# Performance work log

Hardware: AMD Instinct MI355X
Metric: run time of the kernel (lower is better)

Reference implementation:

```python
import jax, jax.numpy as jnp
import numpy as np

B, C, H, W = 32, 256, 64, 64
K = 7  # kernel_size

def setup_inputs() -> dict:
    key = jax.random.key(0)
    kx, kw = jax.random.split(key)
    x = jax.random.normal(kx, (B, C, H, W), dtype=jnp.float32)
    # Conv2d(2, 1, 7, bias=False) weight: [out_ch=1, in_ch=2, 7, 7]
    w = jax.random.normal(kw, (1, 2, K, K), dtype=jnp.float32) * (1.0 / np.sqrt(2 * K * K))
    return {"x": x, "w": w}

def reference(x, w):
    # channel-wise max and mean, keepdim -> [B,1,H,W]
    max_out = jnp.max(x, axis=1, keepdims=True)
    avg_out = jnp.mean(x, axis=1, keepdims=True)
    concat = jnp.concatenate([max_out, avg_out], axis=1)  # [B,2,H,W]
    pad = K // 2
    conv = jax.lax.conv_general_dilated(
        concat, w,
        window_strides=(1, 1),
        padding=[(pad, pad), (pad, pad)],
        dimension_numbers=("NCHW", "OIHW", "NCHW"),
    )  # [B,1,H,W]
    scale = jax.nn.sigmoid(conv)
    return x * scale  # broadcast over channels
```

## Files before the change

kernel.cpp:

```cpp
#include <hip/hip_runtime.h>
#include <math.h>

constexpr int Bn  = 32;
constexpr int Cn  = 256;
constexpr int Hn  = 64;
constexpr int Wn  = 64;
constexpr int HW  = Hn * Wn;
constexpr int CHW = Cn * HW;
constexpr int HW4 = HW / 4;
constexpr int NPOS  = Bn * HW;
constexpr int NPOS4 = NPOS / 4;

constexpr int ROWS   = 16;
constexpr int NSTR   = Hn / ROWS;
constexpr int CGRP   = 16;
constexpr int NCG    = Cn / CGRP;
constexpr int HALO   = 3;
constexpr int LROWS  = ROWS + 2 * HALO;

__global__ __launch_bounds__(256) void reduce_k(const float* __restrict__ x,
                                                float* __restrict__ pmax,
                                                float* __restrict__ pavg) {
    __shared__ float4 smax[4][64];
    __shared__ float4 ssum[4][64];

    const int lane  = threadIdx.x & 63;
    const int chunk = threadIdx.x >> 6;
    const int pos4  = blockIdx.x * 64 + lane;
    const int b     = pos4 >> 10;
    const int sp4   = pos4 & (HW4 - 1);

    const float4* xp = (const float4*)x + (size_t)b * (CHW / 4)
                       + (size_t)(chunk * 64) * HW4 + sp4;

    float4 mx = make_float4(-INFINITY, -INFINITY, -INFINITY, -INFINITY);
    float4 sm = make_float4(0.f, 0.f, 0.f, 0.f);

    #pragma unroll 8
    for (int c = 0; c < 64; ++c) {
        float4 v = xp[(size_t)c * HW4];
        mx.x = fmaxf(mx.x, v.x); mx.y = fmaxf(mx.y, v.y);
        mx.z = fmaxf(mx.z, v.z); mx.w = fmaxf(mx.w, v.w);
        sm.x += v.x; sm.y += v.y; sm.z += v.z; sm.w += v.w;
    }

    smax[chunk][lane] = mx;
    ssum[chunk][lane] = sm;
    __syncthreads();

    if (chunk == 0) {
        float4 M = smax[0][lane];
        float4 S = ssum[0][lane];
        #pragma unroll
        for (int k = 1; k < 4; ++k) {
            float4 m2 = smax[k][lane];
            float4 s2 = ssum[k][lane];
            M.x = fmaxf(M.x, m2.x); M.y = fmaxf(M.y, m2.y);
            M.z = fmaxf(M.z, m2.z); M.w = fmaxf(M.w, m2.w);
            S.x += s2.x; S.y += s2.y; S.z += s2.z; S.w += s2.w;
        }
        const float inv = 1.0f / (float)Cn;
        float4 A = make_float4(S.x * inv, S.y * inv, S.z * inv, S.w * inv);
        ((float4*)pmax)[pos4] = M;
        ((float4*)pavg)[pos4] = A;
    }
}

__global__ __launch_bounds__(256, 8) void convmul_k(const float* __restrict__ x,
                                                    const float* __restrict__ pmax,
                                                    const float* __restrict__ pavg,
                                                    const float* __restrict__ w,
                                                    float* __restrict__ out) {
    __shared__ float spm[LROWS * Wn];
    __shared__ float spa[LROWS * Wn];
    __shared__ float ssc[ROWS * Wn];
    __shared__ float sw[98];

    const int tid = threadIdx.x;
    const int bid = blockIdx.x;
    const int cg     = bid & (NCG - 1);
    const int stripe = (bid >> 4) & (NSTR - 1);
    const int b      = bid >> 6;
    const int r0     = stripe * ROWS;

    if (tid < 98) sw[tid] = w[tid];

    const float* pm = pmax + b * HW;
    const float* pa = pavg + b * HW;
    for (int i = tid; i < LROWS * Wn; i += 256) {
        const int lr  = i >> 6;
        const int col = i & 63;
        const int gh  = r0 - HALO + lr;
        const bool ok = (gh >= 0) && (gh < Hn);
        spm[i] = ok ? pm[gh * Wn + col] : 0.f;
        spa[i] = ok ? pa[gh * Wn + col] : 0.f;
    }
    __syncthreads();

    #pragma unroll
    for (int p = tid; p < ROWS * Wn; p += 256) {
        const int hl  = p >> 6;
        const int col = p & 63;
        float acc = 0.f;
        #pragma unroll
        for (int kh = 0; kh < 7; ++kh) {
            const int lr = hl + kh;
            #pragma unroll
            for (int kw = 0; kw < 7; ++kw) {
                const int ww = col + kw - 3;
                if (ww < 0 || ww >= Wn) continue;
                const int o = lr * Wn + ww;
                acc += spm[o] * sw[kh * 7 + kw] + spa[o] * sw[49 + kh * 7 + kw];
            }
        }
        ssc[p] = 1.f / (1.f + expf(-acc));
    }
    __syncthreads();

    const float4 s = ((const float4*)ssc)[tid];

    const size_t base = (size_t)b * (CHW / 4)
                      + (size_t)(cg * CGRP) * HW4
                      + (size_t)stripe * (ROWS * Wn / 4) + tid;
    const float4* x4 = (const float4*)x;
    float4* o4 = (float4*)out;

    #pragma unroll 4
    for (int ch = 0; ch < CGRP; ++ch) {
        const size_t i4 = base + (size_t)ch * HW4;
        const float4 v = x4[i4];
        float4 o;
        o.x = v.x * s.x; o.y = v.y * s.y;
        o.z = v.z * s.z; o.w = v.w * s.w;
        o4[i4] = o;
    }
}

extern "C" void kernel_launch(void* const* d_in, const int* in_sizes, int n_in,
                              void* d_out, int out_size, void* d_ws, size_t ws_size,
                              hipStream_t stream) {
    const float* x = (const float*)d_in[0];
    const float* w = (const float*)d_in[1];
    float* out = (float*)d_out;

    float* pmax = (float*)d_ws;
    float* pavg = pmax + NPOS;

    reduce_k<<<NPOS4 / 64, 256, 0, stream>>>(x, pmax, pavg);

    convmul_k<<<Bn * NSTR * NCG, 256, 0, stream>>>(x, pmax, pavg, w, out);
}
```

Before: 277.5 us.

## Compute the spatial-attention conv once per position and scale all channels per block

The conv+multiply kernel is repartitioned. Each block now covers 4 rows of one image and all 256 channels, matching reduce_k's tiling, instead of a 16-row stripe times 16 channels. That removes the 16-fold redundant 7x7 conv and sigmoid work across channel groups. The shared-memory halo is padded in the column dimension so the conv loop drops its bounds checks, and output stores become nontemporal. The trade-off is a grid four times smaller with a longer serial channel loop per thread, which may cut the number of memory requests in flight.

```diff
diff --git a/kernel.cpp b/kernel.cpp
--- a/kernel.cpp
+++ b/kernel.cpp
@@ -11,12 +11,12 @@
 constexpr int NPOS  = Bn * HW;
 constexpr int NPOS4 = NPOS / 4;
 
-constexpr int ROWS   = 16;
-constexpr int NSTR   = Hn / ROWS;
-constexpr int CGRP   = 16;
-constexpr int NCG    = Cn / CGRP;
-constexpr int HALO   = 3;
-constexpr int LROWS  = ROWS + 2 * HALO;
+constexpr int CM_ROWS  = 4;
+constexpr int CM_LR    = CM_ROWS + 6;
+constexpr int CM_LC    = 72;
+constexpr int CM_GRID  = NPOS4 / 64;
+
+typedef float f4_t __attribute__((ext_vector_type(4)));
 
 __global__ __launch_bounds__(256) void reduce_k(const float* __restrict__ x,
                                                 float* __restrict__ pmax,
@@ -66,73 +66,72 @@
     }
 }
 
-__global__ __launch_bounds__(256, 8) void convmul_k(const float* __restrict__ x,
-                                                    const float* __restrict__ pmax,
-                                                    const float* __restrict__ pavg,
-                                                    const float* __restrict__ w,
-                                                    float* __restrict__ out) {
-    __shared__ float spm[LROWS * Wn];
-    __shared__ float spa[LROWS * Wn];
-    __shared__ float ssc[ROWS * Wn];
+__global__ __launch_bounds__(256) void convmul_k(const float* __restrict__ x,
+                                                 const float* __restrict__ pmax,
+                                                 const float* __restrict__ pavg,
+                                                 const float* __restrict__ w,
+                                                 float* __restrict__ out) {
+    __shared__ float spm[CM_LR][CM_LC];
+    __shared__ float spa[CM_LR][CM_LC];
+    __shared__ float ssc[256];
     __shared__ float sw[98];
 
     const int tid = threadIdx.x;
     const int bid = blockIdx.x;
-    const int cg     = bid & (NCG - 1);
-    const int stripe = (bid >> 4) & (NSTR - 1);
-    const int b      = bid >> 6;
-    const int r0     = stripe * ROWS;
+    const int b   = bid >> 4;
+    const int rg  = bid & 15;
+    const int row0 = rg * CM_ROWS;
 
     if (tid < 98) sw[tid] = w[tid];
 
     const float* pm = pmax + b * HW;
     const float* pa = pavg + b * HW;
-    for (int i = tid; i < LROWS * Wn; i += 256) {
-        const int lr  = i >> 6;
-        const int col = i & 63;
-        const int gh  = r0 - HALO + lr;
-        const bool ok = (gh >= 0) && (gh < Hn);
-        spm[i] = ok ? pm[gh * Wn + col] : 0.f;
-        spa[i] = ok ? pa[gh * Wn + col] : 0.f;
+    for (int i = tid; i < CM_LR * CM_LC; i += 256) {
+        const int lr = i / CM_LC;
+        const int lc = i % CM_LC;
+        const int gh = row0 - 3 + lr;
+        const int gw = lc - 3;
+        const bool ok = (gh >= 0) && (gh < Hn) && (gw >= 0) && (gw < Wn);
+        const float vm = ok ? pm[gh * Wn + gw] : 0.f;
+        const float va = ok ? pa[gh * Wn + gw] : 0.f;
+        spm[lr][lc] = vm;
+        spa[lr][lc] = va;
     }
     __syncthreads();
 
-    #pragma unroll
-    for (int p = tid; p < ROWS * Wn; p += 256) {
-        const int hl  = p >> 6;
-        const int col = p & 63;
+    {
+        const int hl  = tid >> 6;
+        const int col = tid & 63;
         float acc = 0.f;
         #pragma unroll
         for (int kh = 0; kh < 7; ++kh) {
-            const int lr = hl + kh;
             #pragma unroll
             for (int kw = 0; kw < 7; ++kw) {
-                const int ww = col + kw - 3;
-                if (ww < 0 || ww >= Wn) continue;
-                const int o = lr * Wn + ww;
-                acc += spm[o] * sw[kh * 7 + kw] + spa[o] * sw[49 + kh * 7 + kw];
+                acc += spm[hl + kh][col + kw] * sw[kh * 7 + kw]
+                     + spa[hl + kh][col + kw] * sw[49 + kh * 7 + kw];
             }
         }
-        ssc[p] = 1.f / (1.f + expf(-acc));
+        ssc[tid] = 1.f / (1.f + expf(-acc));
     }
     __syncthreads();
 
-    const float4 s = ((const float4*)ssc)[tid];
+    const int wv   = tid >> 6;
+    const int lane = tid & 63;
+    const int sp4  = rg * 64 + lane;
 
-    const size_t base = (size_t)b * (CHW / 4)
-                      + (size_t)(cg * CGRP) * HW4
-                      + (size_t)stripe * (ROWS * Wn / 4) + tid;
+    const float4 s = ((const float4*)ssc)[lane];
+
     const float4* x4 = (const float4*)x;
     float4* o4 = (float4*)out;
 
+    size_t idx = (size_t)b * (CHW / 4) + (size_t)(wv * 64) * HW4 + sp4;
     #pragma unroll 4
-    for (int ch = 0; ch < CGRP; ++ch) {
-        const size_t i4 = base + (size_t)ch * HW4;
-        const float4 v = x4[i4];
-        float4 o;
+    for (int k = 0; k < 64; ++k, idx += HW4) {
+        const float4 v = x4[idx];
+        f4_t o;
         o.x = v.x * s.x; o.y = v.y * s.y;
         o.z = v.z * s.z; o.w = v.w * s.w;
-        o4[i4] = o;
+        __builtin_nontemporal_store(o, (f4_t*)&o4[idx]);
     }
 }
 
@@ -148,5 +147,5 @@
 
     reduce_k<<<NPOS4 / 64, 256, 0, stream>>>(x, pmax, pavg);
 
-    convmul_k<<<Bn * NSTR * NCG, 256, 0, stream>>>(x, pmax, pavg, w, out);
+    convmul_k<<<CM_GRID, 256, 0, stream>>>(x, pmax, pavg, w, out);
 }
```

After: 248.5 us. 1.12x faster.
